# Optimization experiments

Measured on AMD Instinct MI355X. Metric: run time of the kernel, lower is better.

Reference implementation:

```python
import jax, jax.numpy as jnp
import numpy as np

N = 50000      # total nodes after flattening [1,1,N,D]
E = 600000     # random edges (plus N self-loops appended)
D = 128        # in_dim == out_dim
H = 8          # num_heads
DP = D // H    # per-head dim (each_out_dim)
SLOPE = 0.2    # DGL GATv2Conv default negative_slope


def setup_inputs() -> dict:
    key = jax.random.key(0)
    ks = jax.random.split(key, 6)
    x = jax.random.normal(ks[0], (1, 1, N, D), dtype=jnp.float32)
    s = 1.0 / np.sqrt(D).astype(np.float32)
    # GATv2Conv params: separate src/dst linear projections (share_weights=False),
    # with bias, plus a per-head attention vector.
    w_src = jax.random.uniform(ks[1], (D, H * DP), jnp.float32, -s, s)
    b_src = jnp.zeros((H * DP,), jnp.float32)
    w_dst = jax.random.uniform(ks[2], (D, H * DP), jnp.float32, -s, s)
    b_dst = jnp.zeros((H * DP,), jnp.float32)
    attn_w = jax.random.uniform(ks[3], (H, DP), jnp.float32, -s, s)
    self_loop = jnp.arange(N, dtype=jnp.int32)
    src = jnp.concatenate([jax.random.randint(ks[4], (E,), 0, N, dtype=jnp.int32), self_loop])
    dst = jnp.concatenate([jax.random.randint(ks[5], (E,), 0, N, dtype=jnp.int32), self_loop])
    return {"x": x, "w_src": w_src, "b_src": b_src, "w_dst": w_dst,
            "b_dst": b_dst, "attn_w": attn_w, "src": src, "dst": dst}


def reference(x, w_src, b_src, w_dst, b_dst, attn_w, src, dst):
    shape = x.shape
    h = x.reshape(-1, shape[3])                       # (N, D)
    n = h.shape[0]
    fs = (h @ w_src + b_src).reshape(n, H, DP)        # (N, H, Dp) source proj
    fd = (h @ w_dst + b_dst).reshape(n, H, DP)        # (N, H, Dp) dest proj
    # GATv2: e_ij = a^T LeakyReLU(W_s h_i + W_d h_j)
    e = jax.nn.leaky_relu(fs[src] + fd[dst], SLOPE)   # (E, H, Dp)
    logits = jnp.einsum('ehd,hd->eh', e, attn_w)      # (E, H)
    # segment softmax over incoming edges of each destination node
    m = jax.ops.segment_max(logits, dst, num_segments=n)
    m = jnp.where(jnp.isfinite(m), m, 0.0)
    ex = jnp.exp(logits - m[dst])                     # (E, H)
    denom = jax.ops.segment_sum(ex, dst, num_segments=n)
    alpha = ex / denom[dst]                           # (E, H)
    # weighted scatter-add aggregation of source features
    out = jax.ops.segment_sum(alpha[:, :, None] * fs[src], dst, num_segments=n)
    return out.reshape(shape)
```

## Files before the change

kernel.cpp:

```cpp
#include <hip/hip_runtime.h>
#include <hip/hip_bf16.h>

#define HH 8
#define DP 16
#define DD 128
#define SLOPE 0.2f

#define BM 32
#define COUNT_BLOCKS 512
__global__ __launch_bounds__(256) void proj_count_kernel(
    const float* __restrict__ x,
    const float* __restrict__ w_src, const float* __restrict__ b_src,
    const float* __restrict__ w_dst, const float* __restrict__ b_dst,
    float* __restrict__ fs, float* __restrict__ fd, int n,
    const int* __restrict__ dst, int* __restrict__ count, int ecount) {
  __shared__ float xs[BM][DD];
  const int tid = threadIdx.x;

  if (blockIdx.x < COUNT_BLOCKS) {
    const int stride = COUNT_BLOCKS * 256;
    for (int e = blockIdx.x * 256 + tid; e < ecount; e += stride)
      atomicAdd(&count[dst[e]], 1);
    return;
  }

  const int block0 = (blockIdx.x - COUNT_BLOCKS) * BM;

  for (int i = tid; i < BM * DD / 4; i += 256) {
    int m = i >> 5;
    int k = (i & 31) << 2;
    int node = block0 + m;
    float4 v = make_float4(0.f, 0.f, 0.f, 0.f);
    if (node < n) v = *reinterpret_cast<const float4*>(x + (size_t)node * DD + k);
    *reinterpret_cast<float4*>(&xs[m][k]) = v;
  }
  __syncthreads();

  const int c = tid & (DD - 1);
  const int m0 = (tid >> 7) * 16;

  float acc_s[16], acc_d[16];
#pragma unroll
  for (int m = 0; m < 16; ++m) { acc_s[m] = 0.f; acc_d[m] = 0.f; }

  float ws0 = w_src[0 * DD + c], ws1 = w_src[1 * DD + c];
  float ws2 = w_src[2 * DD + c], ws3 = w_src[3 * DD + c];
  float wd0 = w_dst[0 * DD + c], wd1 = w_dst[1 * DD + c];
  float wd2 = w_dst[2 * DD + c], wd3 = w_dst[3 * DD + c];

  for (int k = 0; k < DD; k += 4) {
    const int kn = (k + 4) & (DD - 1);
    float nws0 = w_src[(kn + 0) * DD + c], nws1 = w_src[(kn + 1) * DD + c];
    float nws2 = w_src[(kn + 2) * DD + c], nws3 = w_src[(kn + 3) * DD + c];
    float nwd0 = w_dst[(kn + 0) * DD + c], nwd1 = w_dst[(kn + 1) * DD + c];
    float nwd2 = w_dst[(kn + 2) * DD + c], nwd3 = w_dst[(kn + 3) * DD + c];
#pragma unroll
    for (int m = 0; m < 16; ++m) {
      float4 xv = *reinterpret_cast<const float4*>(&xs[m0 + m][k]);
      acc_s[m] = fmaf(xv.x, ws0, acc_s[m]);
      acc_s[m] = fmaf(xv.y, ws1, acc_s[m]);
      acc_s[m] = fmaf(xv.z, ws2, acc_s[m]);
      acc_s[m] = fmaf(xv.w, ws3, acc_s[m]);
      acc_d[m] = fmaf(xv.x, wd0, acc_d[m]);
      acc_d[m] = fmaf(xv.y, wd1, acc_d[m]);
      acc_d[m] = fmaf(xv.z, wd2, acc_d[m]);
      acc_d[m] = fmaf(xv.w, wd3, acc_d[m]);
    }
    ws0 = nws0; ws1 = nws1; ws2 = nws2; ws3 = nws3;
    wd0 = nwd0; wd1 = nwd1; wd2 = nwd2; wd3 = nwd3;
  }

  const float bs = b_src[c];
  const float bd = b_dst[c];
#pragma unroll
  for (int m = 0; m < 16; ++m) {
    int node = block0 + m0 + m;
    if (node < n) {
      fs[(size_t)node * DD + c] = acc_s[m] + bs;
      fd[(size_t)node * DD + c] = acc_d[m] + bd;
    }
  }
}

__global__ __launch_bounds__(256) void alloc_kernel(const int* __restrict__ count,
                                                    int* __restrict__ cursor,
                                                    int* __restrict__ total, int n) {
  const int lane = threadIdx.x & 63;
  const int wid = threadIdx.x >> 6;
  const int wave = blockIdx.x * 4 + wid;
  const int i0 = wave * 256;

  int excl[4];
  int carry = 0;
#pragma unroll
  for (int j = 0; j < 4; ++j) {
    int i = i0 + j * 64 + lane;
    int v = (i < n) ? count[i] : 0;
    int incl = v;
#pragma unroll
    for (int off = 1; off < 64; off <<= 1) {
      int t = __shfl_up(incl, (unsigned)off, 64);
      if (lane >= off) incl += t;
    }
    excl[j] = carry + incl - v;
    carry += __shfl(incl, 63, 64);
  }
  int base = 0;
  if (lane == 63) base = atomicAdd(total, carry);
  base = __shfl(base, 63, 64);
#pragma unroll
  for (int j = 0; j < 4; ++j) {
    int i = i0 + j * 64 + lane;
    if (i < n) cursor[i] = base + excl[j];
  }
}

__global__ __launch_bounds__(256) void scatter_kernel(const int* __restrict__ src,
                                                      const int* __restrict__ dst,
                                                      int* __restrict__ cursor,
                                                      int* __restrict__ edge_src, int ecount) {
  int e = blockIdx.x * 256 + threadIdx.x;
  if (e < ecount) {
    int pos = atomicAdd(&cursor[dst[e]], 1);
    edge_src[pos] = src[e];
  }
}

__global__ __launch_bounds__(256) void node_kernel(const float* __restrict__ fs,
                                                   const float* __restrict__ fd,
                                                   const float* __restrict__ attn_w,
                                                   const int* __restrict__ cursor,
                                                   const int* __restrict__ count,
                                                   const int* __restrict__ edge_src,
                                                   float* __restrict__ out, int n) {
  const int wid = threadIdx.x >> 6;
  const int lane = threadIdx.x & 63;
  const int node = blockIdx.x * 4 + wid;
  if (node >= n) return;

  const int d0 = lane * 2;
  const float2 aw = *reinterpret_cast<const float2*>(&attn_w[d0]);
  const float2 fdv = *reinterpret_cast<const float2*>(&fd[(size_t)node * DD + d0]);

  const int e1 = cursor[node];
  const int e0 = e1 - count[node];

  float mx[4] = {-1e30f, -1e30f, -1e30f, -1e30f};
  float den[4] = {0.f, 0.f, 0.f, 0.f};
  float2 ac[4] = {{0.f, 0.f}, {0.f, 0.f}, {0.f, 0.f}, {0.f, 0.f}};

  auto logit_of = [&](float2 fsv) -> float {
    float t0 = fsv.x + fdv.x; t0 = (t0 > 0.f) ? t0 : t0 * SLOPE;
    float t1 = fsv.y + fdv.y; t1 = (t1 > 0.f) ? t1 : t1 * SLOPE;
    float p = aw.x * t0 + aw.y * t1;
    p += __shfl_xor(p, 1, 64);
    p += __shfl_xor(p, 2, 64);
    p += __shfl_xor(p, 4, 64);
    return p;
  };
  auto upd = [](float& m, float& dn, float2& a, float logit, float2 fsv) {
    float mn = fmaxf(m, logit);
    float sc = __expf(m - mn);
    float p = __expf(logit - mn);
    dn = dn * sc + p;
    a.x = a.x * sc + p * fsv.x;
    a.y = a.y * sc + p * fsv.y;
    m = mn;
  };

  int e = e0;
  for (; e + 3 < e1; e += 4) {
    int s0 = edge_src[e], s1 = edge_src[e + 1];
    int s2 = edge_src[e + 2], s3 = edge_src[e + 3];
    float2 f0 = *reinterpret_cast<const float2*>(&fs[(size_t)s0 * DD + d0]);
    float2 f1 = *reinterpret_cast<const float2*>(&fs[(size_t)s1 * DD + d0]);
    float2 f2 = *reinterpret_cast<const float2*>(&fs[(size_t)s2 * DD + d0]);
    float2 f3 = *reinterpret_cast<const float2*>(&fs[(size_t)s3 * DD + d0]);
    float l0 = logit_of(f0), l1 = logit_of(f1);
    float l2 = logit_of(f2), l3 = logit_of(f3);
    upd(mx[0], den[0], ac[0], l0, f0);
    upd(mx[1], den[1], ac[1], l1, f1);
    upd(mx[2], den[2], ac[2], l2, f2);
    upd(mx[3], den[3], ac[3], l3, f3);
  }
  for (; e < e1; ++e) {
    int s0 = edge_src[e];
    float2 f0 = *reinterpret_cast<const float2*>(&fs[(size_t)s0 * DD + d0]);
    float l0 = logit_of(f0);
    upd(mx[0], den[0], ac[0], l0, f0);
  }

  float M = fmaxf(fmaxf(mx[0], mx[1]), fmaxf(mx[2], mx[3]));
  float denom = 0.f, ax = 0.f, ay = 0.f;
#pragma unroll
  for (int j = 0; j < 4; ++j) {
    float s = __expf(mx[j] - M);
    denom += den[j] * s;
    ax += ac[j].x * s;
    ay += ac[j].y * s;
  }

  float inv = (denom > 0.f) ? 1.f / denom : 0.f;
  *reinterpret_cast<float2*>(&out[(size_t)node * DD + d0]) =
      make_float2(ax * inv, ay * inv);
}

extern "C" void kernel_launch(void* const* d_in, const int* in_sizes, int n_in,
                              void* d_out, int out_size, void* d_ws, size_t ws_size,
                              hipStream_t stream) {
  const float* x      = (const float*)d_in[0];
  const float* w_src  = (const float*)d_in[1];
  const float* b_src  = (const float*)d_in[2];
  const float* w_dst  = (const float*)d_in[3];
  const float* b_dst  = (const float*)d_in[4];
  const float* attn_w = (const float*)d_in[5];
  const int* src = (const int*)d_in[6];
  const int* dst = (const int*)d_in[7];
  float* out = (float*)d_out;

  const int n = in_sizes[0] / DD;
  const int ecount = in_sizes[6];

  size_t off = 0;
  float* fs = (float*)((char*)d_ws + off); off += (size_t)n * DD * sizeof(float);
  float* fd = (float*)((char*)d_ws + off); off += (size_t)n * DD * sizeof(float);
  int* edge_src = (int*)((char*)d_ws + off); off += (size_t)ecount * sizeof(int);
  int* cursor   = (int*)((char*)d_ws + off); off += (size_t)n * sizeof(int);
  int* count    = (int*)((char*)d_ws + off); off += (size_t)n * sizeof(int);
  int* total    = (int*)((char*)d_ws + off); off += sizeof(int);
  (void)ws_size;

  hipMemsetAsync(count, 0, (size_t)(n + 1) * sizeof(int), stream);

  const int proj_blocks = (n + BM - 1) / BM;
  proj_count_kernel<<<COUNT_BLOCKS + proj_blocks, 256, 0, stream>>>(
      x, w_src, b_src, w_dst, b_dst, fs, fd, n, dst, count, ecount);
  alloc_kernel<<<(n + 1023) / 1024, 256, 0, stream>>>(count, cursor, total, n);
  scatter_kernel<<<(ecount + 255) / 256, 256, 0, stream>>>(src, dst, cursor, edge_src, ecount);
  node_kernel<<<(n + 3) / 4, 256, 0, stream>>>(fs, fd, attn_w, cursor, count, edge_src, out, n);
}
```

Before: 264.2 us.

## Fold degree counting into projection blocks and software-pipeline edge gathers

Removes the dedicated counting blocks and has every projection block run a strided slice of the destination-degree atomic counting after its GEMM tile. In the node kernel, the feature gathers for the next group of four edges are issued before the current group's logits and online-softmax updates are computed, so memory latency overlaps with arithmetic. This adds register pressure from holding two groups of gathered values. Counting now follows the projection in each block rather than running in separate concurrent blocks.

New measurement: 253.7 us. 1.04x faster.

```diff
diff --git a/kernel.cpp b/kernel.cpp
--- a/kernel.cpp
+++ b/kernel.cpp
@@ -7,7 +7,6 @@
 #define SLOPE 0.2f
 
 #define BM 32
-#define COUNT_BLOCKS 512
 __global__ __launch_bounds__(256) void proj_count_kernel(
     const float* __restrict__ x,
     const float* __restrict__ w_src, const float* __restrict__ b_src,
@@ -16,15 +15,7 @@
     const int* __restrict__ dst, int* __restrict__ count, int ecount) {
   __shared__ float xs[BM][DD];
   const int tid = threadIdx.x;
-
-  if (blockIdx.x < COUNT_BLOCKS) {
-    const int stride = COUNT_BLOCKS * 256;
-    for (int e = blockIdx.x * 256 + tid; e < ecount; e += stride)
-      atomicAdd(&count[dst[e]], 1);
-    return;
-  }
-
-  const int block0 = (blockIdx.x - COUNT_BLOCKS) * BM;
+  const int block0 = blockIdx.x * BM;
 
   for (int i = tid; i < BM * DD / 4; i += 256) {
     int m = i >> 5;
@@ -80,6 +71,11 @@
       fd[(size_t)node * DD + c] = acc_d[m] + bd;
     }
   }
+
+  const int nblocks = (n + BM - 1) / BM;
+  const int stride = nblocks * 256;
+  for (int e = blockIdx.x * 256 + tid; e < ecount; e += stride)
+    atomicAdd(&count[dst[e]], 1);
 }
 
 __global__ __launch_bounds__(256) void alloc_kernel(const int* __restrict__ count,
@@ -167,25 +163,41 @@
     a.y = a.y * sc + p * fsv.y;
     m = mn;
   };
+  auto gather = [&](int s) -> float2 {
+    return *reinterpret_cast<const float2*>(&fs[(size_t)s * DD + d0]);
+  };
 
   int e = e0;
-  for (; e + 3 < e1; e += 4) {
-    int s0 = edge_src[e], s1 = edge_src[e + 1];
-    int s2 = edge_src[e + 2], s3 = edge_src[e + 3];
-    float2 f0 = *reinterpret_cast<const float2*>(&fs[(size_t)s0 * DD + d0]);
-    float2 f1 = *reinterpret_cast<const float2*>(&fs[(size_t)s1 * DD + d0]);
-    float2 f2 = *reinterpret_cast<const float2*>(&fs[(size_t)s2 * DD + d0]);
-    float2 f3 = *reinterpret_cast<const float2*>(&fs[(size_t)s3 * DD + d0]);
+  const int nfull = (e1 - e0) >> 2;
+  if (nfull > 0) {
+    float2 f0 = gather(edge_src[e0]);
+    float2 f1 = gather(edge_src[e0 + 1]);
+    float2 f2 = gather(edge_src[e0 + 2]);
+    float2 f3 = gather(edge_src[e0 + 3]);
+    for (int g = 1; g < nfull; ++g) {
+      const int b = e0 + g * 4;
+      float2 g0 = gather(edge_src[b]);
+      float2 g1 = gather(edge_src[b + 1]);
+      float2 g2 = gather(edge_src[b + 2]);
+      float2 g3 = gather(edge_src[b + 3]);
+      float l0 = logit_of(f0), l1 = logit_of(f1);
+      float l2 = logit_of(f2), l3 = logit_of(f3);
+      upd(mx[0], den[0], ac[0], l0, f0);
+      upd(mx[1], den[1], ac[1], l1, f1);
+      upd(mx[2], den[2], ac[2], l2, f2);
+      upd(mx[3], den[3], ac[3], l3, f3);
+      f0 = g0; f1 = g1; f2 = g2; f3 = g3;
+    }
     float l0 = logit_of(f0), l1 = logit_of(f1);
     float l2 = logit_of(f2), l3 = logit_of(f3);
     upd(mx[0], den[0], ac[0], l0, f0);
     upd(mx[1], den[1], ac[1], l1, f1);
     upd(mx[2], den[2], ac[2], l2, f2);
     upd(mx[3], den[3], ac[3], l3, f3);
+    e = e0 + nfull * 4;
   }
   for (; e < e1; ++e) {
-    int s0 = edge_src[e];
-    float2 f0 = *reinterpret_cast<const float2*>(&fs[(size_t)s0 * DD + d0]);
+    float2 f0 = gather(edge_src[e]);
     float l0 = logit_of(f0);
     upd(mx[0], den[0], ac[0], l0, f0);
   }
@@ -233,7 +245,7 @@
   hipMemsetAsync(count, 0, (size_t)(n + 1) * sizeof(int), stream);
 
   const int proj_blocks = (n + BM - 1) / BM;
-  proj_count_kernel<<<COUNT_BLOCKS + proj_blocks, 256, 0, stream>>>(
+  proj_count_kernel<<<proj_blocks, 256, 0, stream>>>(
       x, w_src, b_src, w_dst, b_dst, fs, fd, n, dst, count, ecount);
   alloc_kernel<<<(n + 1023) / 1024, 256, 0, stream>>>(count, cursor, total, n);
   scatter_kernel<<<(ecount + 255) / 256, 256, 0, stream>>>(src, dst, cursor, edge_src, ecount);
```
